# Optimization experiments

Hardware: AMD Instinct MI355X
Metric: run time of the kernel (lower is better)

Reference implementation:

```python
import jax, jax.numpy as jnp
import numpy as np

N_NODES = 200000
D_IN = 512
HID = 512
D_OUT = 256
B = 1024
SIZES = (25, 10)


def setup_inputs() -> dict:
    key = jax.random.key(0)
    ks = jax.random.split(key, 8)
    x = jax.random.normal(ks[0], (N_NODES, D_IN), dtype=jnp.float32)
    nodes = jax.random.randint(ks[1], (B,), 0, N_NODES)
    neigh1 = jax.random.randint(ks[2], (B * SIZES[0],), 0, N_NODES)
    neigh2 = jax.random.randint(ks[3], (B * SIZES[0] * SIZES[1],), 0, N_NODES)
    # SAGEAggregator weights, stored as [in, out] (torch Linear weight transposed); bias=False
    s = 0.05
    Ws0 = jax.random.normal(ks[4], (D_IN, HID), dtype=jnp.float32) * s
    Wn0 = jax.random.normal(ks[5], (D_IN, HID), dtype=jnp.float32) * s
    Ws1 = jax.random.normal(ks[6], (2 * HID, D_OUT), dtype=jnp.float32) * s
    Wn1 = jax.random.normal(ks[7], (2 * HID, D_OUT), dtype=jnp.float32) * s
    return {"x": x, "nodes": nodes, "neigh1": neigh1, "neigh2": neigh2,
            "Ws0": Ws0, "Wn0": Wn0, "Ws1": Ws1, "Wn1": Wn1}


def _sage_agg(h_self, h_neigh, Ws, Wn, concat):
    # h_self: [M, d], h_neigh: [M, fanout, d] -> mean aggregate then linear transforms
    m = jnp.mean(h_neigh, axis=1)
    a = h_self @ Ws
    b = m @ Wn
    return jnp.concatenate([a, b], axis=-1) if concat else a + b


def reference(x, nodes, neigh1, neigh2, Ws0, Wn0, Ws1, Wn1):
    # gather features for root nodes and sampled 1-hop / 2-hop neighborhoods
    h0 = x[nodes]    # [B, D_IN]
    h1 = x[neigh1]   # [B*25, D_IN]
    h2 = x[neigh2]   # [B*25*10, D_IN]
    d = D_IN
    # layer 0 (concat=True), act=relu, dropout is identity (inference)
    h0 = jax.nn.relu(_sage_agg(h0, h1.reshape(-1, SIZES[0], d), Ws0, Wn0, True))  # [B, 2*HID]
    h1 = jax.nn.relu(_sage_agg(h1, h2.reshape(-1, SIZES[1], d), Ws0, Wn0, True))  # [B*25, 2*HID]
    d2 = 2 * HID
    # layer 1 (last aggregator, concat=False -> sum), no activation
    out = _sage_agg(h0, h1.reshape(-1, SIZES[0], d2), Ws1, Wn1, False)  # [B, D_OUT]
    return out
```

## Files before the change

kernel.cpp:

```cpp
#include <hip/hip_runtime.h>
#include <hip/hip_bf16.h>


#define DEVINL __device__ __forceinline__

typedef __bf16 bf16x8 __attribute__((ext_vector_type(8)));
typedef float f32x4 __attribute__((ext_vector_type(4)));

DEVINL unsigned short f2bf(float f) {
  union { float f; unsigned u; } v; v.f = f;
  unsigned r = v.u + 0x7FFFu + ((v.u >> 16) & 1u);
  return (unsigned short)(r >> 16);
}
DEVINL float bf2f(unsigned short h) {
  union { unsigned u; float f; } v; v.u = ((unsigned)h) << 16;
  return v.f;
}

DEVINL void gload_lds16(const void* g, void* l) {
  __builtin_amdgcn_global_load_lds(
      (const __attribute__((address_space(1))) void*)g,
      (__attribute__((address_space(3))) void*)l, 16, 0, 0);
}

template <int EPI, int BK>
DEVINL void gemm_core(const unsigned short* __restrict__ A, int lda,
                      const unsigned short* __restrict__ Bt, int ldb,
                      int Kc, long tm, long tn, int col0,
                      unsigned short* __restrict__ C1, float* __restrict__ out, int ldc,
                      unsigned short* As, unsigned short* Bs) {
  const int t = threadIdx.x;
  const int w = t >> 6;
  const int l = t & 63;
  const int wm = w >> 1, wn = w & 1;
  f32x4 acc[4][4] = {};
  constexpr int LPR = BK / 8;
  constexpr int RPW = 64 / LPR;
  constexpr int ROUNDS = 128 / (4 * RPW);
  constexpr int NS = BK / 32;
  const int s_r = l / LPR;
  const int s_kc = (l % LPR) * 8;

  for (int kt = 0; kt < Kc; kt += BK) {
    __syncthreads();
    #pragma unroll
    for (int r = 0; r < ROUNDS; ++r) {
      const int chunk = r * (4 * RPW) + w * RPW;
      gload_lds16(A + (size_t)(tm + chunk + s_r) * lda + kt + s_kc, As + chunk * BK);
      gload_lds16(Bt + (size_t)(tn + chunk + s_r) * ldb + kt + s_kc, Bs + chunk * BK);
    }
    __syncthreads();

    bf16x8 af[4][NS], bfr[4][NS];
    const unsigned short* Ab = As + ((size_t)(wm * 64 + (l & 15)) * BK + (l >> 4) * 8);
    const unsigned short* Bb = Bs + ((size_t)(wn * 64 + (l & 15)) * BK + (l >> 4) * 8);
    #pragma unroll
    for (int f = 0; f < 4; ++f)
      #pragma unroll
      for (int s = 0; s < NS; ++s) {
        af[f][s] = *reinterpret_cast<const bf16x8*>(Ab + f * 16 * BK + s * 32);
        bfr[f][s] = *reinterpret_cast<const bf16x8*>(Bb + f * 16 * BK + s * 32);
      }
    #pragma unroll
    for (int s = 0; s < NS; ++s)
      #pragma unroll
      for (int i = 0; i < 4; ++i)
        #pragma unroll
        for (int j = 0; j < 4; ++j)
          acc[i][j] = __builtin_amdgcn_mfma_f32_16x16x32_bf16(af[i][s], bfr[j][s], acc[i][j], 0, 0, 0);
  }

  const int q = l >> 4, cl = l & 15;
  #pragma unroll
  for (int i = 0; i < 4; ++i)
    #pragma unroll
    for (int j = 0; j < 4; ++j)
      #pragma unroll
      for (int r = 0; r < 4; ++r) {
        const long row = tm + wm * 64 + i * 16 + q * 4 + r;
        const long col = col0 + tn + wn * 64 + j * 16 + cl;
        if (EPI == 0) C1[row * 1024 + col] = f2bf(fmaxf(acc[i][j][r], 0.f));
        else          atomicAdd(out + row * ldc + col, acc[i][j][r]);
      }
}

DEVINL void xcd_tile_map(int b, long& tm, long& tn) {
  const int xcd = b & 7, idx = b >> 3;
  tm = (long)(xcd + 8 * (idx >> 2)) * 128;
  tn = (long)(idx & 3) * 128;
}

DEVINL void mean10_row(const float* __restrict__ x, const int* __restrict__ neigh2,
                       unsigned short* __restrict__ Hmall, int row, int tid) {
  int c4 = (tid & 127) << 2;
  float4 acc = {0.f, 0.f, 0.f, 0.f};
  const int* ip = neigh2 + (size_t)row * 10;
  #pragma unroll
  for (int j = 0; j < 10; ++j) {
    const float4 v = *reinterpret_cast<const float4*>(x + (size_t)ip[j] * 512 + c4);
    acc.x += v.x; acc.y += v.y; acc.z += v.z; acc.w += v.w;
  }
  const float s = 0.1f;
  ushort4 o; o.x = f2bf(acc.x * s); o.y = f2bf(acc.y * s);
  o.z = f2bf(acc.z * s); o.w = f2bf(acc.w * s);
  *reinterpret_cast<ushort4*>(Hmall + (size_t)row * 512 + c4) = o;
}

DEVINL void mean25_c1(const unsigned short* __restrict__ C1all,
                      unsigned short* __restrict__ M1, int g, int c) {
  float a0 = 0, a1 = 0, a2 = 0, a3 = 0;
  for (int j = 0; j < 25; ++j) {
    ushort4 v = *reinterpret_cast<const ushort4*>(C1all + ((size_t)g * 25 + j) * 1024 + c);
    a0 += bf2f(v.x); a1 += bf2f(v.y); a2 += bf2f(v.z); a3 += bf2f(v.w);
  }
  const float s = 1.0f / 25.0f;
  ushort4 o; o.x = f2bf(a0 * s); o.y = f2bf(a1 * s); o.z = f2bf(a2 * s); o.w = f2bf(a3 * s);
  *reinterpret_cast<ushort4*>(M1 + (size_t)g * 1024 + c) = o;
}

__global__ __launch_bounds__(256) void phase0_kernel(
    const float* __restrict__ x, const int* __restrict__ neigh1, const int* __restrict__ nodes,
    const float* __restrict__ Ws0, const float* __restrict__ Wn0,
    const float* __restrict__ Ws1, const float* __restrict__ Wn1,
    unsigned short* __restrict__ Hall,
    unsigned short* __restrict__ WT0s, unsigned short* __restrict__ WT0n,
    unsigned short* __restrict__ WT1s, unsigned short* __restrict__ WT1n,
    float* __restrict__ out) {
  const int b = blockIdx.x;
  const int tid = threadIdx.x;
  if (b < 13312) {
    int row = b * 2 + (tid >> 7);
    int src = row < 25600 ? neigh1[row] : nodes[row - 25600];
    int c4 = (tid & 127) << 2;
    const float4 v = *reinterpret_cast<const float4*>(x + (size_t)src * 512 + c4);
    ushort4 o; o.x = f2bf(v.x); o.y = f2bf(v.y); o.z = f2bf(v.z); o.w = f2bf(v.w);
    *reinterpret_cast<ushort4*>(Hall + (size_t)row * 512 + c4) = o;
  } else if (b < 13312 + 4096) {
    int t = (b - 13312) * 256 + tid;
    int region = t >> 18, local = t & 262143;
    const float* W; unsigned short* WT;
    if (region == 0)      { W = Ws0; WT = WT0s; }
    else if (region == 1) { W = Wn0; WT = WT0n; }
    else if (region == 2) { W = Ws1; WT = WT1s; }
    else                  { W = Wn1; WT = WT1n; }
    int k, n, N;
    if (region < 2) { k = local & 511;  n = local >> 9;  N = 512; }
    else            { k = local & 1023; n = local >> 10; N = 256; }
    WT[local] = f2bf(W[(size_t)k * N + n]);
  } else {
    int t = (b - 17408) * 256 + tid;
    reinterpret_cast<float4*>(out)[t] = float4{0.f, 0.f, 0.f, 0.f};
  }
}

__global__ __launch_bounds__(256) void phase1_kernel(
    const float* __restrict__ x, const int* __restrict__ neigh2,
    const unsigned short* __restrict__ Hall, const unsigned short* __restrict__ WT0s,
    unsigned short* __restrict__ Hmall, unsigned short* __restrict__ C1all) {
  __shared__ __align__(16) unsigned short As[128 * 32];
  __shared__ __align__(16) unsigned short Bs[128 * 32];
  const int b = blockIdx.x;
  const int tid = threadIdx.x;
  if (b < 832) {
    long tm, tn;
    xcd_tile_map(b, tm, tn);
    gemm_core<0, 32>(Hall, 512, WT0s, 512, 512, tm, tn, 0, C1all, nullptr, 0, As, Bs);
  } else if (b < 832 + 12800) {
    mean10_row(x, neigh2, Hmall, (b - 832) * 2 + (tid >> 7), tid);
  } else {
    int g = (b - 13632) * 2 + (tid >> 7);
    int c4 = (tid & 127) << 2;
    float a0 = 0, a1 = 0, a2 = 0, a3 = 0;
    for (int j = 0; j < 25; ++j) {
      ushort4 v = *reinterpret_cast<const ushort4*>(Hall + ((size_t)g * 25 + j) * 512 + c4);
      a0 += bf2f(v.x); a1 += bf2f(v.y); a2 += bf2f(v.z); a3 += bf2f(v.w);
    }
    const float s = 1.0f / 25.0f;
    ushort4 o; o.x = f2bf(a0 * s); o.y = f2bf(a1 * s); o.z = f2bf(a2 * s); o.w = f2bf(a3 * s);
    *reinterpret_cast<ushort4*>(Hmall + ((size_t)25600 + g) * 512 + c4) = o;
  }
}

__global__ __launch_bounds__(256) void phase2_kernel(
    const unsigned short* __restrict__ Hmall, const unsigned short* __restrict__ WT0n,
    unsigned short* __restrict__ C1all) {
  __shared__ __align__(16) unsigned short As[128 * 32];
  __shared__ __align__(16) unsigned short Bs[128 * 32];
  long tm, tn;
  xcd_tile_map(blockIdx.x, tm, tn);
  gemm_core<0, 32>(Hmall, 512, WT0n, 512, 512, tm, tn, 512, C1all, nullptr, 0, As, Bs);
}

__global__ __launch_bounds__(256) void phase3_kernel(const unsigned short* __restrict__ C1all,
                                                     unsigned short* __restrict__ M1) {
  int g = blockIdx.x;
  int c4 = threadIdx.x << 2;
  mean25_c1(C1all, M1, g, c4);
}

__global__ __launch_bounds__(256) void gemm1_kernel(
    const unsigned short* __restrict__ C0, const unsigned short* __restrict__ WT1s,
    const unsigned short* __restrict__ M1, const unsigned short* __restrict__ WT1n,
    float* __restrict__ out) {
  __shared__ __align__(16) unsigned short As[128 * 64];
  __shared__ __align__(16) unsigned short Bs[128 * 64];
  const int pass = blockIdx.z >> 2;
  const int k0 = (blockIdx.z & 3) * 256;
  gemm_core<1, 64>((pass ? M1 : C0) + k0, 1024, (pass ? WT1n : WT1s) + k0, 1024, 256,
                   (long)blockIdx.y * 128, (long)blockIdx.x * 128, 0,
                   nullptr, out, 256, As, Bs);
}

extern "C" void kernel_launch(void* const* d_in, const int* in_sizes, int n_in,
                              void* d_out, int out_size, void* d_ws, size_t ws_size,
                              hipStream_t stream) {
  const float* x      = (const float*)d_in[0];
  const int*   nodes  = (const int*)d_in[1];
  const int*   neigh1 = (const int*)d_in[2];
  const int*   neigh2 = (const int*)d_in[3];
  const float* Ws0    = (const float*)d_in[4];
  const float* Wn0    = (const float*)d_in[5];
  const float* Ws1    = (const float*)d_in[6];
  const float* Wn1    = (const float*)d_in[7];
  float* out = (float*)d_out;

  char* p = (char*)d_ws;
  unsigned short* WT0s  = (unsigned short*)p; p += (size_t)512 * 512 * 2;
  unsigned short* WT0n  = (unsigned short*)p; p += (size_t)512 * 512 * 2;
  unsigned short* WT1s  = (unsigned short*)p; p += (size_t)256 * 1024 * 2;
  unsigned short* WT1n  = (unsigned short*)p; p += (size_t)256 * 1024 * 2;
  unsigned short* Hall  = (unsigned short*)p; p += (size_t)26624 * 512 * 2;
  unsigned short* Hmall = (unsigned short*)p; p += (size_t)26624 * 512 * 2;
  unsigned short* C1all = (unsigned short*)p; p += (size_t)26624 * 1024 * 2;
  unsigned short* M1    = (unsigned short*)p; p += (size_t)1024 * 1024 * 2;

  const unsigned short* C0 = C1all + (size_t)25600 * 1024;

  hipLaunchKernelGGL(phase0_kernel, dim3(17664), dim3(256), 0, stream,
                     x, neigh1, nodes, Ws0, Wn0, Ws1, Wn1,
                     Hall, WT0s, WT0n, WT1s, WT1n, out);
  hipLaunchKernelGGL(phase1_kernel, dim3(14144), dim3(256), 0, stream,
                     x, neigh2, Hall, WT0s, Hmall, C1all);
  hipLaunchKernelGGL(phase2_kernel, dim3(832), dim3(256), 0, stream,
                     Hmall, WT0n, C1all);
  hipLaunchKernelGGL(phase3_kernel, dim3(1024), dim3(256), 0, stream, C1all, M1);
  hipLaunchKernelGGL(gemm1_kernel, dim3(2, 8, 8), dim3(256), 0, stream,
                     C0, WT1s, M1, WT1n, out);
}
```

Baseline: 171.4 us.

## Fuse 25-neighbour mean into layer-0 GEMM epilogue via per-wave partial sums

The layer-0 GEMM epilogue no longer writes the full 25600x1024 bf16 hidden matrix for the 1-hop neighbours. Each wave sums relu outputs per group of 25 rows into fp32 partials, using shuffles across lanes, and writes them to a small buffer P. A new kernel finishes the mean from P and runs the C0·WT1s GEMM in the same launch; the M1·WT1n GEMM runs separately. This removes a large intermediate write plus reread. In exchange it adds fp32 partial traffic, extra epilogue arithmetic and one more launch.

```diff
diff --git a/kernel.cpp b/kernel.cpp
--- a/kernel.cpp
+++ b/kernel.cpp
@@ -27,7 +27,8 @@
 DEVINL void gemm_core(const unsigned short* __restrict__ A, int lda,
                       const unsigned short* __restrict__ Bt, int ldb,
                       int Kc, long tm, long tn, int col0,
-                      unsigned short* __restrict__ C1, float* __restrict__ out, int ldc,
+                      unsigned short* __restrict__ C0, float* __restrict__ P,
+                      float* __restrict__ out, int ldc,
                       unsigned short* As, unsigned short* Bs) {
   const int t = threadIdx.x;
   const int w = t >> 6;
@@ -71,17 +72,61 @@
   }
 
   const int q = l >> 4, cl = l & 15;
-  #pragma unroll
-  for (int i = 0; i < 4; ++i)
+  if (EPI == 0) {
+    if (tm < 25600) {
+      const int wmBase = (int)tm + wm * 64;
+      const int g0w = wmBase / 25;
+      float gacc[4][4] = {};
+      #pragma unroll
+      for (int i = 0; i < 4; ++i)
+        #pragma unroll
+        for (int r = 0; r < 4; ++r) {
+          const int gl = (wmBase + i * 16 + q * 4 + r) / 25 - g0w;
+          #pragma unroll
+          for (int j = 0; j < 4; ++j)
+            gacc[j][gl] += fmaxf(acc[i][j][r], 0.f);
+        }
+      #pragma unroll
+      for (int j = 0; j < 4; ++j)
+        #pragma unroll
+        for (int gl = 0; gl < 4; ++gl) {
+          float v = gacc[j][gl];
+          v += __shfl_xor(v, 16);
+          v += __shfl_xor(v, 32);
+          gacc[j][gl] = v;
+        }
+      if (q == 0) {
+        const int wh = wmBase >> 6;
+        #pragma unroll
+        for (int gl = 0; gl < 4; ++gl)
+          #pragma unroll
+          for (int j = 0; j < 4; ++j)
+            P[((size_t)wh * 4 + gl) * 1024 + col0 + tn + wn * 64 + j * 16 + cl] = gacc[j][gl];
+      }
+    } else {
+      #pragma unroll
+      for (int i = 0; i < 4; ++i)
+        #pragma unroll
+        for (int j = 0; j < 4; ++j)
+          #pragma unroll
+          for (int r = 0; r < 4; ++r) {
+            const long row = tm - 25600 + wm * 64 + i * 16 + q * 4 + r;
+            const long col = col0 + tn + wn * 64 + j * 16 + cl;
+            C0[row * 1024 + col] = f2bf(fmaxf(acc[i][j][r], 0.f));
+          }
+    }
+  } else {
     #pragma unroll
-    for (int j = 0; j < 4; ++j)
-      #pragma unroll
-      for (int r = 0; r < 4; ++r) {
-        const long row = tm + wm * 64 + i * 16 + q * 4 + r;
-        const long col = col0 + tn + wn * 64 + j * 16 + cl;
-        if (EPI == 0) C1[row * 1024 + col] = f2bf(fmaxf(acc[i][j][r], 0.f));
-        else          atomicAdd(out + row * ldc + col, acc[i][j][r]);
-      }
+    for (int i = 0; i < 4; ++i)
+      #pragma unroll
+      for (int j = 0; j < 4; ++j)
+        #pragma unroll
+        for (int r = 0; r < 4; ++r) {
+          const long row = tm + wm * 64 + i * 16 + q * 4 + r;
+          const long col = tn + wn * 64 + j * 16 + cl;
+          atomicAdd(out + row * ldc + col, acc[i][j][r]);
+        }
+  }
 }
 
 DEVINL void xcd_tile_map(int b, long& tm, long& tn) {
@@ -104,18 +149,6 @@
   ushort4 o; o.x = f2bf(acc.x * s); o.y = f2bf(acc.y * s);
   o.z = f2bf(acc.z * s); o.w = f2bf(acc.w * s);
   *reinterpret_cast<ushort4*>(Hmall + (size_t)row * 512 + c4) = o;
-}
-
-DEVINL void mean25_c1(const unsigned short* __restrict__ C1all,
-                      unsigned short* __restrict__ M1, int g, int c) {
-  float a0 = 0, a1 = 0, a2 = 0, a3 = 0;
-  for (int j = 0; j < 25; ++j) {
-    ushort4 v = *reinterpret_cast<const ushort4*>(C1all + ((size_t)g * 25 + j) * 1024 + c);
-    a0 += bf2f(v.x); a1 += bf2f(v.y); a2 += bf2f(v.z); a3 += bf2f(v.w);
-  }
-  const float s = 1.0f / 25.0f;
-  ushort4 o; o.x = f2bf(a0 * s); o.y = f2bf(a1 * s); o.z = f2bf(a2 * s); o.w = f2bf(a3 * s);
-  *reinterpret_cast<ushort4*>(M1 + (size_t)g * 1024 + c) = o;
 }
 
 __global__ __launch_bounds__(256) void phase0_kernel(
@@ -156,7 +189,8 @@
 __global__ __launch_bounds__(256) void phase1_kernel(
     const float* __restrict__ x, const int* __restrict__ neigh2,
     const unsigned short* __restrict__ Hall, const unsigned short* __restrict__ WT0s,
-    unsigned short* __restrict__ Hmall, unsigned short* __restrict__ C1all) {
+    unsigned short* __restrict__ Hmall,
+    unsigned short* __restrict__ C0, float* __restrict__ P) {
   __shared__ __align__(16) unsigned short As[128 * 32];
   __shared__ __align__(16) unsigned short Bs[128 * 32];
   const int b = blockIdx.x;
@@ -164,7 +198,7 @@
   if (b < 832) {
     long tm, tn;
     xcd_tile_map(b, tm, tn);
-    gemm_core<0, 32>(Hall, 512, WT0s, 512, 512, tm, tn, 0, C1all, nullptr, 0, As, Bs);
+    gemm_core<0, 32>(Hall, 512, WT0s, 512, 512, tm, tn, 0, C0, P, nullptr, 0, As, Bs);
   } else if (b < 832 + 12800) {
     mean10_row(x, neigh2, Hmall, (b - 832) * 2 + (tid >> 7), tid);
   } else {
@@ -183,32 +217,53 @@
 
 __global__ __launch_bounds__(256) void phase2_kernel(
     const unsigned short* __restrict__ Hmall, const unsigned short* __restrict__ WT0n,
-    unsigned short* __restrict__ C1all) {
+    unsigned short* __restrict__ C0, float* __restrict__ P) {
   __shared__ __align__(16) unsigned short As[128 * 32];
   __shared__ __align__(16) unsigned short Bs[128 * 32];
   long tm, tn;
   xcd_tile_map(blockIdx.x, tm, tn);
-  gemm_core<0, 32>(Hmall, 512, WT0n, 512, 512, tm, tn, 512, C1all, nullptr, 0, As, Bs);
-}
-
-__global__ __launch_bounds__(256) void phase3_kernel(const unsigned short* __restrict__ C1all,
-                                                     unsigned short* __restrict__ M1) {
-  int g = blockIdx.x;
-  int c4 = threadIdx.x << 2;
-  mean25_c1(C1all, M1, g, c4);
-}
-
-__global__ __launch_bounds__(256) void gemm1_kernel(
+  gemm_core<0, 32>(Hmall, 512, WT0n, 512, 512, tm, tn, 512, C0, P, nullptr, 0, As, Bs);
+}
+
+__global__ __launch_bounds__(256) void phaseD_kernel(
+    const float* __restrict__ P, unsigned short* __restrict__ M1,
     const unsigned short* __restrict__ C0, const unsigned short* __restrict__ WT1s,
+    float* __restrict__ out) {
+  __shared__ __align__(16) unsigned short As[128 * 64];
+  __shared__ __align__(16) unsigned short Bs[128 * 64];
+  const int b = blockIdx.x;
+  if (b < 1024) {
+    const int g = b;
+    const int c = threadIdx.x << 2;
+    const int r0 = g * 25, r1 = g * 25 + 24;
+    const int wh0 = r0 >> 6, wh1 = r1 >> 6;
+    f32x4 s = {0.f, 0.f, 0.f, 0.f};
+    for (int wh = wh0; wh <= wh1; ++wh) {
+      const int slot = g - (wh * 64) / 25;
+      const f32x4 v = *reinterpret_cast<const f32x4*>(P + ((size_t)wh * 4 + slot) * 1024 + c);
+      s[0] += v[0]; s[1] += v[1]; s[2] += v[2]; s[3] += v[3];
+    }
+    const float sc = 1.0f / 25.0f;
+    ushort4 o; o.x = f2bf(s[0] * sc); o.y = f2bf(s[1] * sc);
+    o.z = f2bf(s[2] * sc); o.w = f2bf(s[3] * sc);
+    *reinterpret_cast<ushort4*>(M1 + (size_t)g * 1024 + c) = o;
+  } else {
+    const int u = b - 1024;
+    const int z = u >> 4, bm = (u >> 1) & 7, bn = u & 1;
+    gemm_core<1, 64>(C0 + z * 256, 1024, WT1s + z * 256, 1024, 256,
+                     (long)bm * 128, (long)bn * 128, 0, nullptr, nullptr, out, 256, As, Bs);
+  }
+}
+
+__global__ __launch_bounds__(256) void phaseE_kernel(
     const unsigned short* __restrict__ M1, const unsigned short* __restrict__ WT1n,
     float* __restrict__ out) {
   __shared__ __align__(16) unsigned short As[128 * 64];
   __shared__ __align__(16) unsigned short Bs[128 * 64];
-  const int pass = blockIdx.z >> 2;
-  const int k0 = (blockIdx.z & 3) * 256;
-  gemm_core<1, 64>((pass ? M1 : C0) + k0, 1024, (pass ? WT1n : WT1s) + k0, 1024, 256,
-                   (long)blockIdx.y * 128, (long)blockIdx.x * 128, 0,
-                   nullptr, out, 256, As, Bs);
+  const int b = blockIdx.x;
+  const int z = b >> 4, bm = (b >> 1) & 7, bn = b & 1;
+  gemm_core<1, 64>(M1 + z * 256, 1024, WT1n + z * 256, 1024, 256,
+                   (long)bm * 128, (long)bn * 128, 0, nullptr, nullptr, out, 256, As, Bs);
 }
 
 extern "C" void kernel_launch(void* const* d_in, const int* in_sizes, int n_in,
@@ -231,19 +286,19 @@
   unsigned short* WT1n  = (unsigned short*)p; p += (size_t)256 * 1024 * 2;
   unsigned short* Hall  = (unsigned short*)p; p += (size_t)26624 * 512 * 2;
   unsigned short* Hmall = (unsigned short*)p; p += (size_t)26624 * 512 * 2;
-  unsigned short* C1all = (unsigned short*)p; p += (size_t)26624 * 1024 * 2;
+  unsigned short* C0    = (unsigned short*)p; p += (size_t)1024 * 1024 * 2;
   unsigned short* M1    = (unsigned short*)p; p += (size_t)1024 * 1024 * 2;
-
-  const unsigned short* C0 = C1all + (size_t)25600 * 1024;
+  float*          P     = (float*)p;          p += (size_t)400 * 4 * 1024 * 4;
 
   hipLaunchKernelGGL(phase0_kernel, dim3(17664), dim3(256), 0, stream,
                      x, neigh1, nodes, Ws0, Wn0, Ws1, Wn1,
                      Hall, WT0s, WT0n, WT1s, WT1n, out);
   hipLaunchKernelGGL(phase1_kernel, dim3(14144), dim3(256), 0, stream,
-                     x, neigh2, Hall, WT0s, Hmall, C1all);
+                     x, neigh2, Hall, WT0s, Hmall, C0, P);
   hipLaunchKernelGGL(phase2_kernel, dim3(832), dim3(256), 0, stream,
-                     Hmall, WT0n, C1all);
-  hipLaunchKernelGGL(phase3_kernel, dim3(1024), dim3(256), 0, stream, C1all, M1);
-  hipLaunchKernelGGL(gemm1_kernel, dim3(2, 8, 8), dim3(256), 0, stream,
-                     C0, WT1s, M1, WT1n, out);
-}
+                     Hmall, WT0n, C0, P);
+  hipLaunchKernelGGL(phaseD_kernel, dim3(1088), dim3(256), 0, stream,
+                     P, M1, C0, WT1s, out);
+  hipLaunchKernelGGL(phaseE_kernel, dim3(64), dim3(256), 0, stream,
+                     M1, WT1n, out);
+}
```

Measured after the change: 185.0 us. +8.0%, slower.
